# Optimization experiments

Hardware: AMD Instinct MI355X
Metric: run time of the kernel (lower is better)

Reference implementation:

```python
import jax, jax.numpy as jnp
import numpy as np

N, NFEAT, NHID, NH2, NCLASS = 16384, 512, 256, 64, 10


def setup_inputs() -> dict:
    key = jax.random.key(0)
    ks = jax.random.split(key, 12)
    x = jax.random.normal(ks[0], (N, NFEAT), dtype=jnp.float32)
    # dense (row-normalized-style) adjacency; sparsified to ~avg degree 32
    a = jax.random.uniform(ks[1], (N, N), dtype=jnp.float32)
    mask = (jax.random.uniform(ks[2], (N, N)) < (32.0 / N)).astype(jnp.float32)
    adj = a * mask / 32.0
    s = lambda fin: 1.0 / np.sqrt(fin)
    W1 = jax.random.uniform(ks[3], (NFEAT, NHID), jnp.float32, -s(NFEAT), s(NFEAT))
    b1 = jax.random.uniform(ks[4], (NHID,), jnp.float32, -s(NFEAT), s(NFEAT))
    W2 = jax.random.uniform(ks[5], (NHID, NH2), jnp.float32, -s(NHID), s(NHID))
    b2 = jax.random.uniform(ks[6], (NH2,), jnp.float32, -s(NHID), s(NHID))
    W3 = jax.random.uniform(ks[7], (NH2, 32), jnp.float32, -s(NH2), s(NH2))
    b3 = jax.random.uniform(ks[8], (32,), jnp.float32, -s(NH2), s(NH2))
    W4 = jax.random.uniform(ks[9], (32, 16), jnp.float32, -s(32), s(32))
    b4 = jax.random.uniform(ks[10], (16,), jnp.float32, -s(32), s(32))
    W5 = jax.random.uniform(ks[11], (16, NCLASS), jnp.float32, -s(16), s(16))
    b5 = jnp.zeros((NCLASS,), jnp.float32)
    return {"x": x, "adj": adj, "W1": W1, "b1": b1, "W2": W2, "b2": b2,
            "W3": W3, "b3": b3, "W4": W4, "b4": b4, "W5": W5, "b5": b5}


def reference(x, adj, W1, b1, W2, b2, W3, b3, W4, b4, W5, b5):
    # GraphConvolution: adj @ (x @ W) + b
    h = jax.nn.relu(adj @ (x @ W1) + b1)          # [N, NHID]
    h = adj @ (h @ W2) + b2                        # [N, 64]
    g = jnp.max(h, axis=0)                         # [64] graph max-pool
    g = jax.nn.relu(g @ W3 + b3)                   # [32]
    g = jax.nn.relu(g @ W4 + b4)                   # [16]
    return g @ W5 + b5                             # [NCLASS]
```

## Files before the change

kernel.cpp:

```cpp
#include <hip/hip_runtime.h>
#include <hip/hip_bf16.h>
#include <cstdint>

#define NROW 16384
#define NFEAT 512
#define NHID 256
#define NH2 64
#define CAP 96

typedef float vfloat4 __attribute__((ext_vector_type(4)));

#define BM 128
#define BN 64
#define BK 16

__global__ __launch_bounds__(256, 4) void kA_gemm(
    const float* __restrict__ X, const float* __restrict__ W1,
    float* __restrict__ XW1) {
  __shared__ float As[BK][BM + 4];
  __shared__ float Bs[BK][BN];
  const int t = threadIdx.x;
  const int bm = (blockIdx.x >> 2) * BM;
  const int bn = (blockIdx.x & 3) * BN;
  const int tx = t & 15;
  const int ty = t >> 4;
  const int ar = t >> 1;
  const int ak = (t & 1) * 8;
  const int bk = t >> 4;
  const int bnn = (t & 15) * 4;
  float acc[8][4] = {};
  for (int k0 = 0; k0 < NFEAT; k0 += BK) {
    const float4 a0 = *(const float4*)&X[(size_t)(bm + ar) * NFEAT + k0 + ak];
    const float4 a1 = *(const float4*)&X[(size_t)(bm + ar) * NFEAT + k0 + ak + 4];
    const float4 b0 = *(const float4*)&W1[(size_t)(k0 + bk) * NHID + bn + bnn];
    As[ak + 0][ar] = a0.x; As[ak + 1][ar] = a0.y;
    As[ak + 2][ar] = a0.z; As[ak + 3][ar] = a0.w;
    As[ak + 4][ar] = a1.x; As[ak + 5][ar] = a1.y;
    As[ak + 6][ar] = a1.z; As[ak + 7][ar] = a1.w;
    *(float4*)&Bs[bk][bnn] = b0;
    __syncthreads();
#pragma unroll
    for (int k = 0; k < BK; ++k) {
      float a[8], b[4];
#pragma unroll
      for (int i = 0; i < 8; ++i) a[i] = As[k][ty * 8 + i];
#pragma unroll
      for (int j = 0; j < 4; ++j) b[j] = Bs[k][tx * 4 + j];
#pragma unroll
      for (int i = 0; i < 8; ++i)
#pragma unroll
        for (int j = 0; j < 4; ++j) acc[i][j] += a[i] * b[j];
    }
    __syncthreads();
  }
#pragma unroll
  for (int i = 0; i < 8; ++i) {
    float4 v = {acc[i][0], acc[i][1], acc[i][2], acc[i][3]};
    *(float4*)&XW1[(size_t)(bm + ty * 8 + i) * NHID + bn + tx * 4] = v;
  }
}

__global__ __launch_bounds__(256, 6) void kB_stream_prop1(
    const float* __restrict__ adj, const float* __restrict__ XW1,
    const float* __restrict__ b1, const float* __restrict__ W2,
    float* __restrict__ vals, int* __restrict__ cols, int* __restrict__ cnt,
    float* __restrict__ H1W2) {
  __shared__ int   scl[4][CAP];
  __shared__ float sv[4][CAP];
  __shared__ float sh[4][NHID];
  __shared__ float sp[4][256];
  const int t = threadIdx.x;
  const int w = t >> 6, lane = t & 63;
  const int row0 = blockIdx.x * 4;
  const int row = row0 + w;

  const float* arow = adj + (size_t)row * NROW;
  int count = 0;
  vfloat4 buf[4];
#pragma unroll
  for (int j = 0; j < 4; ++j)
    buf[j] = __builtin_nontemporal_load((const vfloat4*)&arow[j * 256 + lane * 4]);
  for (int c0 = 0; c0 < NROW; c0 += 1024) {
    vfloat4 cur[4];
#pragma unroll
    for (int j = 0; j < 4; ++j) cur[j] = buf[j];
    if (c0 + 1024 < NROW) {
#pragma unroll
      for (int j = 0; j < 4; ++j)
        buf[j] = __builtin_nontemporal_load(
            (const vfloat4*)&arow[c0 + 1024 + j * 256 + lane * 4]);
    }
#pragma unroll
    for (int j = 0; j < 4; ++j) {
#pragma unroll
      for (int k = 0; k < 4; ++k) {
        const float val = cur[j][k];
        const unsigned long long m = __ballot(val != 0.0f);
        if (val != 0.0f) {
          const int pos = count + __popcll(m & ((1ull << lane) - 1ull));
          if (pos < CAP) { sv[w][pos] = val; scl[w][pos] = c0 + j * 256 + lane * 4 + k; }
        }
        count += __popcll(m);
      }
    }
  }
  const int n = count < CAP ? count : CAP;
  if (lane == 0) cnt[row] = n;
  for (int j = lane; j < n; j += 64) {
    cols[(size_t)row * CAP + j] = scl[w][j];
    vals[(size_t)row * CAP + j] = sv[w][j];
  }

  float4 a0 = {0,0,0,0}, a1 = {0,0,0,0}, a2 = {0,0,0,0}, a3 = {0,0,0,0};
  int k = 0;
  for (; k + 4 <= n; k += 4) {
    const float v0 = sv[w][k], v1 = sv[w][k+1], v2 = sv[w][k+2], v3 = sv[w][k+3];
    const int   c0i = scl[w][k], c1i = scl[w][k+1], c2i = scl[w][k+2], c3i = scl[w][k+3];
    const float4 x0 = *(const float4*)&XW1[(size_t)c0i * NHID + lane * 4];
    const float4 x1 = *(const float4*)&XW1[(size_t)c1i * NHID + lane * 4];
    const float4 x2 = *(const float4*)&XW1[(size_t)c2i * NHID + lane * 4];
    const float4 x3 = *(const float4*)&XW1[(size_t)c3i * NHID + lane * 4];
    a0.x += v0*x0.x; a0.y += v0*x0.y; a0.z += v0*x0.z; a0.w += v0*x0.w;
    a1.x += v1*x1.x; a1.y += v1*x1.y; a1.z += v1*x1.z; a1.w += v1*x1.w;
    a2.x += v2*x2.x; a2.y += v2*x2.y; a2.z += v2*x2.z; a2.w += v2*x2.w;
    a3.x += v3*x3.x; a3.y += v3*x3.y; a3.z += v3*x3.z; a3.w += v3*x3.w;
  }
  for (; k < n; ++k) {
    const float v0 = sv[w][k];
    const float4 x0 = *(const float4*)&XW1[(size_t)scl[w][k] * NHID + lane * 4];
    a0.x += v0*x0.x; a0.y += v0*x0.y; a0.z += v0*x0.z; a0.w += v0*x0.w;
  }
  const float4 bb = *(const float4*)&b1[lane * 4];
  float4 h;
  h.x = fmaxf(a0.x + a1.x + a2.x + a3.x + bb.x, 0.f);
  h.y = fmaxf(a0.y + a1.y + a2.y + a3.y + bb.y, 0.f);
  h.z = fmaxf(a0.z + a1.z + a2.z + a3.z + bb.z, 0.f);
  h.w = fmaxf(a0.w + a1.w + a2.w + a3.w + bb.w, 0.f);
  *(float4*)&sh[w][lane * 4] = h;
  __syncthreads();

  const int c = t & 63, q = t >> 6;
  float p0 = 0.f, p1 = 0.f, p2 = 0.f, p3 = 0.f;
#pragma unroll 8
  for (int kk = 0; kk < 64; ++kk) {
    const int kidx = q * 64 + kk;
    const float wv = W2[kidx * NH2 + c];
    p0 += sh[0][kidx] * wv;
    p1 += sh[1][kidx] * wv;
    p2 += sh[2][kidx] * wv;
    p3 += sh[3][kidx] * wv;
  }
  sp[0][t] = p0; sp[1][t] = p1; sp[2][t] = p2; sp[3][t] = p3;
  __syncthreads();
  {
    const int r2 = t >> 6, c2 = t & 63;
    H1W2[(size_t)(row0 + r2) * NH2 + c2] =
        sp[r2][c2] + sp[r2][c2 + 64] + sp[r2][c2 + 128] + sp[r2][c2 + 192];
  }
}

__global__ __launch_bounds__(256, 6) void kC_prop2(
    const float* __restrict__ H1W2, const float* __restrict__ vals,
    const int* __restrict__ cols, const int* __restrict__ cnt,
    const float* __restrict__ b2, float* __restrict__ blockmax) {
  __shared__ int   scl[4][CAP];
  __shared__ float sv[4][CAP];
  __shared__ float smax[4][NH2];
  const int t = threadIdx.x;
  const int w = t >> 6, l = t & 63;
  const int row = blockIdx.x * 4 + w;
  const int n = cnt[row];
  for (int jj = l; jj < n; jj += 64) {
    scl[w][jj] = cols[(size_t)row * CAP + jj];
    sv[w][jj]  = vals[(size_t)row * CAP + jj];
  }
  __syncthreads();
  float a0 = 0.f, a1 = 0.f, a2 = 0.f, a3 = 0.f;
  int k = 0;
  for (; k + 4 <= n; k += 4) {
    a0 += sv[w][k + 0] * H1W2[(size_t)scl[w][k + 0] * NH2 + l];
    a1 += sv[w][k + 1] * H1W2[(size_t)scl[w][k + 1] * NH2 + l];
    a2 += sv[w][k + 2] * H1W2[(size_t)scl[w][k + 2] * NH2 + l];
    a3 += sv[w][k + 3] * H1W2[(size_t)scl[w][k + 3] * NH2 + l];
  }
  for (; k < n; ++k) a0 += sv[w][k] * H1W2[(size_t)scl[w][k] * NH2 + l];
  smax[w][l] = a0 + a1 + a2 + a3 + b2[l];
  __syncthreads();
  if (t < NH2) {
    const float m = fmaxf(fmaxf(smax[0][t], smax[1][t]),
                          fmaxf(smax[2][t], smax[3][t]));
    blockmax[(size_t)blockIdx.x * NH2 + t] = m;
  }
}

__global__ __launch_bounds__(256) void kD1_colmax(const float* __restrict__ blockmax,
                                                  float* __restrict__ partial) {
  __shared__ float sm[256];
  const int t = threadIdx.x, c = t & 63, q = t >> 6;
  const int base = blockIdx.x * 64;
  float m = -3.4e38f;
  for (int r = q; r < 64; r += 4)
    m = fmaxf(m, blockmax[(size_t)(base + r) * NH2 + c]);
  sm[t] = m;
  __syncthreads();
  if (t < 64)
    partial[blockIdx.x * 64 + t] =
        fmaxf(fmaxf(sm[t], sm[t + 64]), fmaxf(sm[t + 128], sm[t + 192]));
}

__global__ __launch_bounds__(64) void kD2_final(const float* __restrict__ partial,
                                                const float* __restrict__ W3,
                                                const float* __restrict__ b3,
                                                const float* __restrict__ W4,
                                                const float* __restrict__ b4,
                                                const float* __restrict__ W5,
                                                const float* __restrict__ b5,
                                                float* __restrict__ out) {
  __shared__ float g[64], t3[32], t4[16];
  const int t = threadIdx.x;
  float m = -3.4e38f;
  for (int p = 0; p < 64; ++p) m = fmaxf(m, partial[p * 64 + t]);
  g[t] = m;
  __syncthreads();
  if (t < 32) {
    float acc = b3[t];
    for (int k = 0; k < 64; ++k) acc += g[k] * W3[k * 32 + t];
    t3[t] = acc > 0.f ? acc : 0.f;
  }
  __syncthreads();
  if (t < 16) {
    float acc = b4[t];
    for (int k = 0; k < 32; ++k) acc += t3[k] * W4[k * 16 + t];
    t4[t] = acc > 0.f ? acc : 0.f;
  }
  __syncthreads();
  if (t < 10) {
    float acc = b5[t];
    for (int k = 0; k < 16; ++k) acc += t4[k] * W5[k * 10 + t];
    out[t] = acc;
  }
}

extern "C" void kernel_launch(void* const* d_in, const int* in_sizes, int n_in,
                              void* d_out, int out_size, void* d_ws, size_t ws_size,
                              hipStream_t stream) {
  const float* x   = (const float*)d_in[0];
  const float* adj = (const float*)d_in[1];
  const float* W1  = (const float*)d_in[2];
  const float* b1  = (const float*)d_in[3];
  const float* W2  = (const float*)d_in[4];
  const float* b2  = (const float*)d_in[5];
  const float* W3  = (const float*)d_in[6];
  const float* b3  = (const float*)d_in[7];
  const float* W4  = (const float*)d_in[8];
  const float* b4  = (const float*)d_in[9];
  const float* W5  = (const float*)d_in[10];
  const float* b5  = (const float*)d_in[11];
  float* out = (float*)d_out;

  char* ws = (char*)d_ws;
  float* XW1      = (float*)(ws);
  float* vals     = (float*)(ws + (size_t)16 * 1024 * 1024);
  int*   cols     = (int*)  (ws + (size_t)24 * 1024 * 1024);
  int*   cnt      = (int*)  (ws + (size_t)32 * 1024 * 1024);
  float* H1W2     = (float*)(ws + (size_t)36 * 1024 * 1024);
  float* blockmax = (float*)(ws + (size_t)40 * 1024 * 1024);
  float* partial  = (float*)(ws + (size_t)44 * 1024 * 1024);

  kA_gemm<<<512, 256, 0, stream>>>(x, W1, XW1);
  kB_stream_prop1<<<NROW / 4, 256, 0, stream>>>(adj, XW1, b1, W2,
                                                vals, cols, cnt, H1W2);
  kC_prop2<<<NROW / 4, 256, 0, stream>>>(H1W2, vals, cols, cnt, b2, blockmax);
  kD1_colmax<<<64, 256, 0, stream>>>(blockmax, partial);
  kD2_final<<<1, 64, 0, stream>>>(partial, W3, b3, W4, b4, W5, b5, out);
}
```

Baseline: 1.452 ms.

## Overlap X@W1 GEMM with adjacency compaction in one interleaved launch

Merges the X@W1 GEMM and the dense adjacency scan into one kernel. GEMM blocks are interleaved with stream blocks in the first 1024 block IDs, so the compute-bound GEMM runs alongside the memory-bound 1 GB adjacency read. The compaction writes cols/vals directly to global memory and skips 256-column chunks that are entirely zero using a wave-wide ballot pre-check. A new gather kernel reloads the compacted lists into shared memory before the XW1 propagation. This costs an extra launch and a global round trip for the sparse lists, and the GEMM blocks use launch bounds of 4 instead of 6 for the streaming work.

```diff
diff --git a/kernel.cpp b/kernel.cpp
--- a/kernel.cpp
+++ b/kernel.cpp
@@ -14,56 +14,108 @@
 #define BN 64
 #define BK 16
 
-__global__ __launch_bounds__(256, 4) void kA_gemm(
+__global__ __launch_bounds__(256, 4) void kAB_gemm_stream(
     const float* __restrict__ X, const float* __restrict__ W1,
-    float* __restrict__ XW1) {
+    float* __restrict__ XW1, const float* __restrict__ adj,
+    float* __restrict__ vals, int* __restrict__ cols, int* __restrict__ cnt) {
   __shared__ float As[BK][BM + 4];
   __shared__ float Bs[BK][BN];
   const int t = threadIdx.x;
-  const int bm = (blockIdx.x >> 2) * BM;
-  const int bn = (blockIdx.x & 3) * BN;
-  const int tx = t & 15;
-  const int ty = t >> 4;
-  const int ar = t >> 1;
-  const int ak = (t & 1) * 8;
-  const int bk = t >> 4;
-  const int bnn = (t & 15) * 4;
-  float acc[8][4] = {};
-  for (int k0 = 0; k0 < NFEAT; k0 += BK) {
-    const float4 a0 = *(const float4*)&X[(size_t)(bm + ar) * NFEAT + k0 + ak];
-    const float4 a1 = *(const float4*)&X[(size_t)(bm + ar) * NFEAT + k0 + ak + 4];
-    const float4 b0 = *(const float4*)&W1[(size_t)(k0 + bk) * NHID + bn + bnn];
-    As[ak + 0][ar] = a0.x; As[ak + 1][ar] = a0.y;
-    As[ak + 2][ar] = a0.z; As[ak + 3][ar] = a0.w;
-    As[ak + 4][ar] = a1.x; As[ak + 5][ar] = a1.y;
-    As[ak + 6][ar] = a1.z; As[ak + 7][ar] = a1.w;
-    *(float4*)&Bs[bk][bnn] = b0;
-    __syncthreads();
-#pragma unroll
-    for (int k = 0; k < BK; ++k) {
-      float a[8], b[4];
-#pragma unroll
-      for (int i = 0; i < 8; ++i) a[i] = As[k][ty * 8 + i];
-#pragma unroll
-      for (int j = 0; j < 4; ++j) b[j] = Bs[k][tx * 4 + j];
-#pragma unroll
-      for (int i = 0; i < 8; ++i)
-#pragma unroll
-        for (int j = 0; j < 4; ++j) acc[i][j] += a[i] * b[j];
-    }
-    __syncthreads();
-  }
-#pragma unroll
-  for (int i = 0; i < 8; ++i) {
-    float4 v = {acc[i][0], acc[i][1], acc[i][2], acc[i][3]};
-    *(float4*)&XW1[(size_t)(bm + ty * 8 + i) * NHID + bn + tx * 4] = v;
-  }
-}
-
-__global__ __launch_bounds__(256, 6) void kB_stream_prop1(
-    const float* __restrict__ adj, const float* __restrict__ XW1,
-    const float* __restrict__ b1, const float* __restrict__ W2,
-    float* __restrict__ vals, int* __restrict__ cols, int* __restrict__ cnt,
+  const int sid = blockIdx.x;
+
+  if (sid < 1024 && (sid & 1)) {
+    const int gid = sid >> 1;
+    const int bm = (gid >> 2) * BM;
+    const int bn = (gid & 3) * BN;
+    const int tx = t & 15;
+    const int ty = t >> 4;
+    const int ar = t >> 1;
+    const int ak = (t & 1) * 8;
+    const int bk = t >> 4;
+    const int bnn = (t & 15) * 4;
+    float acc[8][4] = {};
+    for (int k0 = 0; k0 < NFEAT; k0 += BK) {
+      const float4 a0 = *(const float4*)&X[(size_t)(bm + ar) * NFEAT + k0 + ak];
+      const float4 a1 = *(const float4*)&X[(size_t)(bm + ar) * NFEAT + k0 + ak + 4];
+      const float4 b0 = *(const float4*)&W1[(size_t)(k0 + bk) * NHID + bn + bnn];
+      As[ak + 0][ar] = a0.x; As[ak + 1][ar] = a0.y;
+      As[ak + 2][ar] = a0.z; As[ak + 3][ar] = a0.w;
+      As[ak + 4][ar] = a1.x; As[ak + 5][ar] = a1.y;
+      As[ak + 6][ar] = a1.z; As[ak + 7][ar] = a1.w;
+      *(float4*)&Bs[bk][bnn] = b0;
+      __syncthreads();
+#pragma unroll
+      for (int k = 0; k < BK; ++k) {
+        float a[8], b[4];
+#pragma unroll
+        for (int i = 0; i < 8; ++i) a[i] = As[k][ty * 8 + i];
+#pragma unroll
+        for (int j = 0; j < 4; ++j) b[j] = Bs[k][tx * 4 + j];
+#pragma unroll
+        for (int i = 0; i < 8; ++i)
+#pragma unroll
+          for (int j = 0; j < 4; ++j) acc[i][j] += a[i] * b[j];
+      }
+      __syncthreads();
+    }
+#pragma unroll
+    for (int i = 0; i < 8; ++i) {
+      float4 v = {acc[i][0], acc[i][1], acc[i][2], acc[i][3]};
+      *(float4*)&XW1[(size_t)(bm + ty * 8 + i) * NHID + bn + tx * 4] = v;
+    }
+    return;
+  }
+
+  const int rid = (sid < 1024) ? (sid >> 1) : (sid - 512);
+  const int w = t >> 6, lane = t & 63;
+  const int row = rid * 4 + w;
+  const float* arow = adj + (size_t)row * NROW;
+  int count = 0;
+  vfloat4 buf[4];
+#pragma unroll
+  for (int j = 0; j < 4; ++j)
+    buf[j] = __builtin_nontemporal_load((const vfloat4*)&arow[j * 256 + lane * 4]);
+  for (int c0 = 0; c0 < NROW; c0 += 1024) {
+    vfloat4 cur[4];
+#pragma unroll
+    for (int j = 0; j < 4; ++j) cur[j] = buf[j];
+    if (c0 + 1024 < NROW) {
+#pragma unroll
+      for (int j = 0; j < 4; ++j)
+        buf[j] = __builtin_nontemporal_load(
+            (const vfloat4*)&arow[c0 + 1024 + j * 256 + lane * 4]);
+    }
+#pragma unroll
+    for (int j = 0; j < 4; ++j) {
+      const vfloat4 v = cur[j];
+      const unsigned long long anym =
+          __ballot((v[0] != 0.0f) || (v[1] != 0.0f) ||
+                   (v[2] != 0.0f) || (v[3] != 0.0f));
+      if (anym == 0ull) continue;
+#pragma unroll
+      for (int k = 0; k < 4; ++k) {
+        const float val = v[k];
+        const unsigned long long m = __ballot(val != 0.0f);
+        if (val != 0.0f) {
+          const int pre = __builtin_amdgcn_mbcnt_hi(
+              (uint32_t)(m >> 32), __builtin_amdgcn_mbcnt_lo((uint32_t)m, 0u));
+          const int pos = count + pre;
+          if (pos < CAP) {
+            cols[(size_t)row * CAP + pos] = c0 + j * 256 + lane * 4 + k;
+            vals[(size_t)row * CAP + pos] = val;
+          }
+        }
+        count += (int)__popcll(m);
+      }
+    }
+  }
+  if (lane == 0) cnt[row] = count < CAP ? count : CAP;
+}
+
+__global__ __launch_bounds__(256, 6) void kB2_gather_w2(
+    const float* __restrict__ XW1, const float* __restrict__ b1,
+    const float* __restrict__ W2, const float* __restrict__ vals,
+    const int* __restrict__ cols, const int* __restrict__ cnt,
     float* __restrict__ H1W2) {
   __shared__ int   scl[4][CAP];
   __shared__ float sv[4][CAP];
@@ -73,43 +125,12 @@
   const int w = t >> 6, lane = t & 63;
   const int row0 = blockIdx.x * 4;
   const int row = row0 + w;
-
-  const float* arow = adj + (size_t)row * NROW;
-  int count = 0;
-  vfloat4 buf[4];
-#pragma unroll
-  for (int j = 0; j < 4; ++j)
-    buf[j] = __builtin_nontemporal_load((const vfloat4*)&arow[j * 256 + lane * 4]);
-  for (int c0 = 0; c0 < NROW; c0 += 1024) {
-    vfloat4 cur[4];
-#pragma unroll
-    for (int j = 0; j < 4; ++j) cur[j] = buf[j];
-    if (c0 + 1024 < NROW) {
-#pragma unroll
-      for (int j = 0; j < 4; ++j)
-        buf[j] = __builtin_nontemporal_load(
-            (const vfloat4*)&arow[c0 + 1024 + j * 256 + lane * 4]);
-    }
-#pragma unroll
-    for (int j = 0; j < 4; ++j) {
-#pragma unroll
-      for (int k = 0; k < 4; ++k) {
-        const float val = cur[j][k];
-        const unsigned long long m = __ballot(val != 0.0f);
-        if (val != 0.0f) {
-          const int pos = count + __popcll(m & ((1ull << lane) - 1ull));
-          if (pos < CAP) { sv[w][pos] = val; scl[w][pos] = c0 + j * 256 + lane * 4 + k; }
-        }
-        count += __popcll(m);
-      }
-    }
-  }
-  const int n = count < CAP ? count : CAP;
-  if (lane == 0) cnt[row] = n;
+  const int n = cnt[row];
   for (int j = lane; j < n; j += 64) {
-    cols[(size_t)row * CAP + j] = scl[w][j];
-    vals[(size_t)row * CAP + j] = sv[w][j];
-  }
+    scl[w][j] = cols[(size_t)row * CAP + j];
+    sv[w][j]  = vals[(size_t)row * CAP + j];
+  }
+  __syncthreads();
 
   float4 a0 = {0,0,0,0}, a1 = {0,0,0,0}, a2 = {0,0,0,0}, a3 = {0,0,0,0};
   int k = 0;
@@ -267,9 +288,8 @@
   float* blockmax = (float*)(ws + (size_t)40 * 1024 * 1024);
   float* partial  = (float*)(ws + (size_t)44 * 1024 * 1024);
 
-  kA_gemm<<<512, 256, 0, stream>>>(x, W1, XW1);
-  kB_stream_prop1<<<NROW / 4, 256, 0, stream>>>(adj, XW1, b1, W2,
-                                                vals, cols, cnt, H1W2);
+  kAB_gemm_stream<<<4608, 256, 0, stream>>>(x, W1, XW1, adj, vals, cols, cnt);
+  kB2_gather_w2<<<NROW / 4, 256, 0, stream>>>(XW1, b1, W2, vals, cols, cnt, H1W2);
   kC_prop2<<<NROW / 4, 256, 0, stream>>>(H1W2, vals, cols, cnt, b2, blockmax);
   kD1_colmax<<<64, 256, 0, stream>>>(blockmax, partial);
   kD2_final<<<1, 64, 0, stream>>>(partial, W3, b3, W4, b4, W5, b5, out);
```

Result: slower. 1.496 ms (+3.0%).
